# Kernel optimization log

Measured on AMD Instinct MI355X. Metric: run time of the kernel, lower is better.

## Reference

```python
import jax, jax.numpy as jnp
import numpy as np

N_NODES = 100000
N_EDGES = 1600000
D = 128  # h_feats


def setup_inputs() -> dict:
    key = jax.random.key(0)
    k1, k2, k3, k4 = jax.random.split(key, 4)
    x = jax.random.normal(k1, (N_NODES, D), dtype=jnp.float32)
    edge_index = jax.random.randint(k2, (2, N_EDGES), 0, N_NODES, dtype=jnp.int64)
    # Linear(2D -> D), torch layout [out, in]
    W1 = jax.random.normal(k3, (D, 2 * D), dtype=jnp.float32) * (1.0 / np.sqrt(2 * D))
    b1 = jnp.zeros((D,), dtype=jnp.float32)
    # Linear(D -> 1)
    W2 = jax.random.normal(k4, (1, D), dtype=jnp.float32) * (1.0 / np.sqrt(D))
    b2 = jnp.zeros((1,), dtype=jnp.float32)
    return {"x": x, "edge_index": edge_index, "W1": W1, "b1": b1, "W2": W2, "b2": b2}


def reference(x, edge_index, W1, b1, W2, b2):
    # gather both endpoints and concat along features: [E, 2D]
    h = jnp.concatenate([x[edge_index[0]], x[edge_index[1]]], axis=-1)
    h = jax.nn.relu(h @ W1.T + b1)          # [E, D]
    h = h @ W2.T + b2                        # [E, 1]
    return h.squeeze(1)                      # [E]
```

## Files before the change

### kernel.cpp

```cpp
#include <hip/hip_runtime.h>
#include <hip/hip_bf16.h>

#define N_NODES 100000
#define N_EDGES 1600000
#define NT_TILES 1563
#define PRE_BLKX 392

#define BQ_OFF 12800000
#define SA_OFF 25600000
#define SB_OFF 26000000

typedef __attribute__((ext_vector_type(8))) short short8v;
typedef __attribute__((ext_vector_type(4))) float float4v;

__device__ __forceinline__ unsigned short f2bf(float f) {
    unsigned int u = __float_as_uint(f);
    u += 0x7fffu + ((u >> 16) & 1u);
    return (unsigned short)(u >> 16);
}
__device__ __forceinline__ unsigned int pack2bf(float a, float b) {
    return (unsigned int)f2bf(a) | ((unsigned int)f2bf(b) << 16);
}
__device__ __forceinline__ float2 bfpair(unsigned int w) {
    return float2{__uint_as_float(w << 16), __uint_as_float(w & 0xffff0000u)};
}
#define MAGICB 12583040.0f
__device__ __forceinline__ unsigned int qmagic(float f, float inv) {
    return __float_as_uint(fmaf(f, inv, MAGICB));
}

__global__ __launch_bounds__(256) void precompute_kernel(
    const float* __restrict__ x, const float* __restrict__ W1,
    const float* __restrict__ b1, unsigned char* __restrict__ Aq,
    unsigned char* __restrict__ Bq, float* __restrict__ sA,
    float* __restrict__ sB) {
    __shared__ unsigned short wlds[128 * 136];
    __shared__ unsigned short xlds[64 * 136];

    const int tid = threadIdx.x;
    const int by = blockIdx.y;
    unsigned char* __restrict__ Q = by ? Bq : Aq;
    float* __restrict__ S = by ? sB : sA;

    const int wave = tid >> 6;
    const int lane = tid & 63;
    const int quad = lane >> 4;
    const int l15 = lane & 15;

    float4 b1v[2];
#pragma unroll
    for (int j = 0; j < 2; ++j)
        b1v[j] = *reinterpret_cast<const float4*>(b1 + wave * 32 + j * 16 + quad * 4);

#pragma unroll
    for (int i = 0; i < 16; ++i) {
        int fi = tid + i * 256;
        int jl = fi >> 5, c4 = fi & 31;
        float4 w4 = reinterpret_cast<const float4*>(W1)[(size_t)jl * 64 + by * 32 + c4];
        unsigned int* d = reinterpret_cast<unsigned int*>(&wlds[jl * 136 + c4 * 4]);
        d[0] = pack2bf(w4.x, w4.y);
        d[1] = pack2bf(w4.z, w4.w);
    }

    float4 xr[8];
    int t = blockIdx.x;
#pragma unroll
    for (int i = 0; i < 8; ++i) {
        int fi = tid + i * 256;
        int n = fi >> 5, c4 = fi & 31;
        int nn = t * 64 + n; nn = nn < N_NODES ? nn : N_NODES - 1;
        xr[i] = reinterpret_cast<const float4*>(x)[(size_t)nn * 32 + c4];
    }

    for (; t < NT_TILES; t += PRE_BLKX) {
        __syncthreads();
#pragma unroll
        for (int i = 0; i < 8; ++i) {
            int fi = tid + i * 256;
            int n = fi >> 5, c4 = fi & 31;
            unsigned int* d = reinterpret_cast<unsigned int*>(&xlds[n * 136 + c4 * 4]);
            d[0] = pack2bf(xr[i].x, xr[i].y);
            d[1] = pack2bf(xr[i].z, xr[i].w);
        }
        __syncthreads();

        const int tn = t + PRE_BLKX;
        if (tn < NT_TILES) {
#pragma unroll
            for (int i = 0; i < 8; ++i) {
                int fi = tid + i * 256;
                int n = fi >> 5, c4 = fi & 31;
                int nn = tn * 64 + n; nn = nn < N_NODES ? nn : N_NODES - 1;
                xr[i] = reinterpret_cast<const float4*>(x)[(size_t)nn * 32 + c4];
            }
        }

        float4v acc[4][2];
#pragma unroll
        for (int i = 0; i < 4; ++i)
#pragma unroll
            for (int j = 0; j < 2; ++j) acc[i][j] = float4v{0.f, 0.f, 0.f, 0.f};

#pragma unroll
        for (int s = 0; s < 4; ++s) {
            const int k0 = s * 32 + quad * 8;
            short8v wf[2], xf[4];
#pragma unroll
            for (int j = 0; j < 2; ++j)
                wf[j] = *reinterpret_cast<const short8v*>(&wlds[(wave * 32 + j * 16 + l15) * 136 + k0]);
#pragma unroll
            for (int i = 0; i < 4; ++i)
                xf[i] = *reinterpret_cast<const short8v*>(&xlds[(i * 16 + l15) * 136 + k0]);
#pragma unroll
            for (int i = 0; i < 4; ++i)
#pragma unroll
                for (int j = 0; j < 2; ++j)
                    acc[i][j] = __builtin_amdgcn_mfma_f32_16x16x32_bf16(wf[j], xf[i], acc[i][j], 0, 0, 0);
        }
        __syncthreads();

#pragma unroll
        for (int i = 0; i < 4; ++i) {
            const int nl = i * 16 + l15;
#pragma unroll
            for (int j = 0; j < 2; ++j) {
                const int colb = wave * 32 + j * 16 + quad * 4;
                float r0 = acc[i][j][0], r1 = acc[i][j][1];
                float r2 = acc[i][j][2], r3 = acc[i][j][3];
                if (by == 0) {
                    r0 += b1v[j].x; r1 += b1v[j].y;
                    r2 += b1v[j].z; r3 += b1v[j].w;
                }
                uint2 st = {pack2bf(r0, r1), pack2bf(r2, r3)};
                *reinterpret_cast<uint2*>(&xlds[nl * 132 + colb]) = st;
            }
        }
        __syncthreads();

        const int row = tid >> 2, part = tid & 3;
        const int n = t * 64 + row;
        uint4 wv[4];
#pragma unroll
        for (int q = 0; q < 4; ++q)
            wv[q] = *reinterpret_cast<const uint4*>(&xlds[row * 132 + part * 32 + q * 8]);

        float m = 1e-6f;
#pragma unroll
        for (int q = 0; q < 4; ++q) {
            unsigned int ws[4] = {wv[q].x, wv[q].y, wv[q].z, wv[q].w};
#pragma unroll
            for (int w = 0; w < 4; ++w) {
                float2 f = bfpair(ws[w]);
                m = fmaxf(m, fmaxf(fabsf(f.x), fabsf(f.y)));
            }
        }
        m = fmaxf(m, __shfl_xor(m, 1));
        m = fmaxf(m, __shfl_xor(m, 2));
        const float inv = 127.0f / m;

        unsigned int ob[8];
#pragma unroll
        for (int q = 0; q < 4; ++q) {
            unsigned int ws[4] = {wv[q].x, wv[q].y, wv[q].z, wv[q].w};
#pragma unroll
            for (int w = 0; w < 2; ++w) {
                float2 f0 = bfpair(ws[2 * w + 0]);
                float2 f1 = bfpair(ws[2 * w + 1]);
                unsigned int q0 = qmagic(f0.x, inv), q1 = qmagic(f0.y, inv);
                unsigned int q2 = qmagic(f1.x, inv), q3 = qmagic(f1.y, inv);
                ob[q * 2 + w] = (q0 & 0xffu) | ((q1 & 0xffu) << 8) |
                                ((q2 & 0xffu) << 16) | (q3 << 24);
            }
        }
        if (n < N_NODES) {
            uint4 s0 = {ob[0], ob[1], ob[2], ob[3]};
            uint4 s1 = {ob[4], ob[5], ob[6], ob[7]};
            uint4* dst = reinterpret_cast<uint4*>(Q + (size_t)n * 128 + part * 32);
            dst[0] = s0;
            dst[1] = s1;
            if (part == 0) S[n] = m * (1.0f / 127.0f);
        }
    }
}

template <bool IS64>
__device__ __forceinline__ void edge_loop(
    const long long* __restrict__ ei, const unsigned char* __restrict__ Aq,
    const unsigned char* __restrict__ Bq, const float* __restrict__ sA,
    const float* __restrict__ sB, const float* __restrict__ W2, float bias2,
    float* __restrict__ out, int wid, int nwaves, int eg, int sl) {
    const int k0 = sl * 32;
    float w2f[32];
#pragma unroll
    for (int j = 0; j < 8; ++j)
        *reinterpret_cast<float4*>(&w2f[j * 4]) =
            *reinterpret_cast<const float4*>(W2 + k0 + j * 4);
    const int* e32 = reinterpret_cast<const int*>(ei);

    for (int base = wid * 16; base < N_EDGES; base += nwaves * 16) {
        const int e = base + eg;
        int u, v;
        if (IS64) { u = (int)ei[e]; v = (int)ei[N_EDGES + e]; }
        else      { u = e32[e];     v = e32[N_EDGES + e]; }

        const uint4* pa = reinterpret_cast<const uint4*>(Aq + (unsigned)u * 128 + k0);
        const uint4* pb = reinterpret_cast<const uint4*>(Bq + (unsigned)v * 128 + k0);
        uint4 a0 = pa[0], a1 = pa[1];
        uint4 b0 = pb[0], b1w = pb[1];
        const float su = sA[u];
        const float sv = sB[v];
        const float r = sv * __builtin_amdgcn_rcpf(su);
        const float c = fmaf(r, 128.0f, 128.0f);

        unsigned int aw[8] = {a0.x, a0.y, a0.z, a0.w, a1.x, a1.y, a1.z, a1.w};
        unsigned int bw[8] = {b0.x, b0.y, b0.z, b0.w, b1w.x, b1w.y, b1w.z, b1w.w};

        float p = 0.f;
#pragma unroll
        for (int wi = 0; wi < 8; ++wi) {
#pragma unroll
            for (int byt = 0; byt < 4; ++byt) {
                float fa = (float)((aw[wi] >> (8 * byt)) & 0xffu);
                float fb = (float)((bw[wi] >> (8 * byt)) & 0xffu);
                float s = fmaxf(fmaf(fb, r, fa) - c, 0.f);
                p = fmaf(s, w2f[wi * 4 + byt], p);
            }
        }
        p += __shfl_xor(p, 1);
        p += __shfl_xor(p, 2);
        if (sl == 0) out[e] = fmaf(su, p, bias2);
    }
}

__global__ __launch_bounds__(256, 8) void edge_kernel(
    const long long* __restrict__ ei, const unsigned char* __restrict__ Aq,
    const unsigned char* __restrict__ Bq, const float* __restrict__ sA,
    const float* __restrict__ sB, const float* __restrict__ W2,
    const float* __restrict__ b2, float* __restrict__ out) {
    const int lane = threadIdx.x & 63;
    const int eg = lane >> 2;
    const int sl = lane & 3;
    const float bias2 = b2[0];

    const unsigned int hi = reinterpret_cast<const unsigned int*>(ei)[2 * lane + 1];
    const bool is64 = (__ballot(hi != 0) == 0ull);

    const int wid = (int)(((unsigned)(blockIdx.x * blockDim.x + threadIdx.x)) >> 6);
    const int nwaves = (int)(((unsigned)(gridDim.x * blockDim.x)) >> 6);

    if (is64) edge_loop<true>(ei, Aq, Bq, sA, sB, W2, bias2, out, wid, nwaves, eg, sl);
    else      edge_loop<false>(ei, Aq, Bq, sA, sB, W2, bias2, out, wid, nwaves, eg, sl);
}

extern "C" void kernel_launch(void* const* d_in, const int* in_sizes, int n_in,
                              void* d_out, int out_size, void* d_ws, size_t ws_size,
                              hipStream_t stream) {
    const float* x = (const float*)d_in[0];
    const long long* ei = (const long long*)d_in[1];
    const float* W1 = (const float*)d_in[2];
    const float* b1 = (const float*)d_in[3];
    const float* W2 = (const float*)d_in[4];
    const float* b2 = (const float*)d_in[5];
    float* out = (float*)d_out;

    unsigned char* Aq = (unsigned char*)d_ws;
    unsigned char* Bq = (unsigned char*)d_ws + BQ_OFF;
    float* sA = (float*)((char*)d_ws + SA_OFF);
    float* sB = (float*)((char*)d_ws + SB_OFF);

    dim3 g1(PRE_BLKX, 2);
    precompute_kernel<<<g1, 256, 0, stream>>>(x, W1, b1, Aq, Bq, sA, sB);
    edge_kernel<<<2048, 256, 0, stream>>>(ei, Aq, Bq, sA, sB, W2, b2, out);
}
```

Before: 182.3 us.

## Fuse A/B node projections into one block per 32-node tile

The precompute kernel now computes both halves of W1 (the source and destination projections) in one block over 32-node tiles, instead of two grid rows that each reload the same x tile. Each x tile is read from global memory once and feeds 256 output columns, with each wave owning 64 columns. Quantisation is factored into a helper that runs twice per tile, sharing the LDS staging buffer. The cost is a 64KB weight LDS footprint, which limits occupancy, plus extra barriers. The edge kernel's launch-bounds occupancy hint also drops from 8 to 4.

```diff
diff --git a/kernel.cpp b/kernel.cpp
--- a/kernel.cpp
+++ b/kernel.cpp
@@ -3,8 +3,8 @@
 
 #define N_NODES 100000
 #define N_EDGES 1600000
-#define NT_TILES 1563
-#define PRE_BLKX 392
+#define NT32    3125
+#define PRE_BLKS 625
 
 #define BQ_OFF 12800000
 #define SA_OFF 25600000
@@ -27,6 +27,40 @@
 #define MAGICB 12583040.0f
 __device__ __forceinline__ unsigned int qmagic(float f, float inv) {
     return __float_as_uint(fmaf(f, inv, MAGICB));
+}
+
+__device__ __forceinline__ void quant_store(
+    const unsigned short* __restrict__ xlds, unsigned char* __restrict__ Q,
+    float* __restrict__ S, int n0, int tid) {
+    const int row = tid >> 3, part = tid & 7;
+    const unsigned short* src = xlds + row * 132 + part * 16;
+    uint4 w0 = *reinterpret_cast<const uint4*>(src);
+    uint4 w1 = *reinterpret_cast<const uint4*>(src + 8);
+    unsigned int ws[8] = {w0.x, w0.y, w0.z, w0.w, w1.x, w1.y, w1.z, w1.w};
+    float m = 1e-6f;
+#pragma unroll
+    for (int k = 0; k < 8; ++k) {
+        float2 f = bfpair(ws[k]);
+        m = fmaxf(m, fmaxf(fabsf(f.x), fabsf(f.y)));
+    }
+    m = fmaxf(m, __shfl_xor(m, 1));
+    m = fmaxf(m, __shfl_xor(m, 2));
+    m = fmaxf(m, __shfl_xor(m, 4));
+    const float inv = 127.0f / m;
+    unsigned int ob[4];
+#pragma unroll
+    for (int k = 0; k < 4; ++k) {
+        float2 f0 = bfpair(ws[2 * k]);
+        float2 f1 = bfpair(ws[2 * k + 1]);
+        unsigned int q0 = qmagic(f0.x, inv), q1 = qmagic(f0.y, inv);
+        unsigned int q2 = qmagic(f1.x, inv), q3 = qmagic(f1.y, inv);
+        ob[k] = (q0 & 0xffu) | ((q1 & 0xffu) << 8) |
+                ((q2 & 0xffu) << 16) | (q3 << 24);
+    }
+    const int n = n0 + row;
+    *reinterpret_cast<uint4*>(Q + (size_t)n * 128 + part * 16) =
+        uint4{ob[0], ob[1], ob[2], ob[3]};
+    if (part == 0) S[n] = m * (1.0f / 127.0f);
 }
 
 __global__ __launch_bounds__(256) void precompute_kernel(
@@ -34,152 +68,118 @@
     const float* __restrict__ b1, unsigned char* __restrict__ Aq,
     unsigned char* __restrict__ Bq, float* __restrict__ sA,
     float* __restrict__ sB) {
-    __shared__ unsigned short wlds[128 * 136];
-    __shared__ unsigned short xlds[64 * 136];
+    __shared__ unsigned short wlds[256 * 132];
+    __shared__ unsigned short xlds[32 * 132];
 
     const int tid = threadIdx.x;
-    const int by = blockIdx.y;
-    unsigned char* __restrict__ Q = by ? Bq : Aq;
-    float* __restrict__ S = by ? sB : sA;
-
-    const int wave = tid >> 6;
-    const int lane = tid & 63;
-    const int quad = lane >> 4;
-    const int l15 = lane & 15;
-
-    float4 b1v[2];
-#pragma unroll
-    for (int j = 0; j < 2; ++j)
-        b1v[j] = *reinterpret_cast<const float4*>(b1 + wave * 32 + j * 16 + quad * 4);
-
-#pragma unroll
-    for (int i = 0; i < 16; ++i) {
+    const int wave = tid >> 6, lane = tid & 63;
+    const int quad = lane >> 4, l15 = lane & 15;
+
+    float4 b1v[4];
+    if (wave < 2) {
+#pragma unroll
+        for (int j = 0; j < 4; ++j)
+            b1v[j] = *reinterpret_cast<const float4*>(b1 + wave * 64 + j * 16 + quad * 4);
+    }
+
+#pragma unroll
+    for (int i = 0; i < 32; ++i) {
         int fi = tid + i * 256;
-        int jl = fi >> 5, c4 = fi & 31;
-        float4 w4 = reinterpret_cast<const float4*>(W1)[(size_t)jl * 64 + by * 32 + c4];
-        unsigned int* d = reinterpret_cast<unsigned int*>(&wlds[jl * 136 + c4 * 4]);
+        int jc = fi >> 5, c4 = fi & 31;
+        float4 w4 = reinterpret_cast<const float4*>(
+            W1)[(size_t)(jc & 127) * 64 + (jc >> 7) * 32 + c4];
+        unsigned int* d = reinterpret_cast<unsigned int*>(&wlds[jc * 132 + c4 * 4]);
         d[0] = pack2bf(w4.x, w4.y);
         d[1] = pack2bf(w4.z, w4.w);
     }
 
-    float4 xr[8];
+    float4 xr[4];
     int t = blockIdx.x;
 #pragma unroll
-    for (int i = 0; i < 8; ++i) {
+    for (int i = 0; i < 4; ++i) {
         int fi = tid + i * 256;
         int n = fi >> 5, c4 = fi & 31;
-        int nn = t * 64 + n; nn = nn < N_NODES ? nn : N_NODES - 1;
-        xr[i] = reinterpret_cast<const float4*>(x)[(size_t)nn * 32 + c4];
-    }
-
-    for (; t < NT_TILES; t += PRE_BLKX) {
-        __syncthreads();
-#pragma unroll
-        for (int i = 0; i < 8; ++i) {
+        xr[i] = reinterpret_cast<const float4*>(x)[(size_t)(t * 32 + n) * 32 + c4];
+    }
+
+    for (; t < NT32; t += PRE_BLKS) {
+        __syncthreads();
+#pragma unroll
+        for (int i = 0; i < 4; ++i) {
             int fi = tid + i * 256;
             int n = fi >> 5, c4 = fi & 31;
-            unsigned int* d = reinterpret_cast<unsigned int*>(&xlds[n * 136 + c4 * 4]);
+            unsigned int* d = reinterpret_cast<unsigned int*>(&xlds[n * 132 + c4 * 4]);
             d[0] = pack2bf(xr[i].x, xr[i].y);
             d[1] = pack2bf(xr[i].z, xr[i].w);
         }
         __syncthreads();
 
-        const int tn = t + PRE_BLKX;
-        if (tn < NT_TILES) {
-#pragma unroll
-            for (int i = 0; i < 8; ++i) {
+        const int tn = t + PRE_BLKS;
+        if (tn < NT32) {
+#pragma unroll
+            for (int i = 0; i < 4; ++i) {
                 int fi = tid + i * 256;
                 int n = fi >> 5, c4 = fi & 31;
-                int nn = tn * 64 + n; nn = nn < N_NODES ? nn : N_NODES - 1;
-                xr[i] = reinterpret_cast<const float4*>(x)[(size_t)nn * 32 + c4];
+                xr[i] = reinterpret_cast<const float4*>(x)[(size_t)(tn * 32 + n) * 32 + c4];
             }
         }
 
-        float4v acc[4][2];
-#pragma unroll
-        for (int i = 0; i < 4; ++i)
-#pragma unroll
-            for (int j = 0; j < 2; ++j) acc[i][j] = float4v{0.f, 0.f, 0.f, 0.f};
+        float4v acc[2][4];
+#pragma unroll
+        for (int i = 0; i < 2; ++i)
+#pragma unroll
+            for (int j = 0; j < 4; ++j) acc[i][j] = float4v{0.f, 0.f, 0.f, 0.f};
 
 #pragma unroll
         for (int s = 0; s < 4; ++s) {
             const int k0 = s * 32 + quad * 8;
-            short8v wf[2], xf[4];
-#pragma unroll
-            for (int j = 0; j < 2; ++j)
-                wf[j] = *reinterpret_cast<const short8v*>(&wlds[(wave * 32 + j * 16 + l15) * 136 + k0]);
-#pragma unroll
-            for (int i = 0; i < 4; ++i)
-                xf[i] = *reinterpret_cast<const short8v*>(&xlds[(i * 16 + l15) * 136 + k0]);
-#pragma unroll
-            for (int i = 0; i < 4; ++i)
-#pragma unroll
-                for (int j = 0; j < 2; ++j)
+            short8v xf[2], wf[4];
+#pragma unroll
+            for (int i = 0; i < 2; ++i)
+                xf[i] = *reinterpret_cast<const short8v*>(&xlds[(i * 16 + l15) * 132 + k0]);
+#pragma unroll
+            for (int j = 0; j < 4; ++j)
+                wf[j] = *reinterpret_cast<const short8v*>(
+                    &wlds[(wave * 64 + j * 16 + l15) * 132 + k0]);
+#pragma unroll
+            for (int i = 0; i < 2; ++i)
+#pragma unroll
+                for (int j = 0; j < 4; ++j)
                     acc[i][j] = __builtin_amdgcn_mfma_f32_16x16x32_bf16(wf[j], xf[i], acc[i][j], 0, 0, 0);
         }
         __syncthreads();
 
-#pragma unroll
-        for (int i = 0; i < 4; ++i) {
-            const int nl = i * 16 + l15;
-#pragma unroll
-            for (int j = 0; j < 2; ++j) {
-                const int colb = wave * 32 + j * 16 + quad * 4;
-                float r0 = acc[i][j][0], r1 = acc[i][j][1];
-                float r2 = acc[i][j][2], r3 = acc[i][j][3];
-                if (by == 0) {
-                    r0 += b1v[j].x; r1 += b1v[j].y;
-                    r2 += b1v[j].z; r3 += b1v[j].w;
+        if (wave < 2) {
+#pragma unroll
+            for (int i = 0; i < 2; ++i)
+#pragma unroll
+                for (int j = 0; j < 4; ++j) {
+                    const int col = wave * 64 + j * 16 + quad * 4;
+                    float r0 = acc[i][j][0] + b1v[j].x;
+                    float r1 = acc[i][j][1] + b1v[j].y;
+                    float r2 = acc[i][j][2] + b1v[j].z;
+                    float r3 = acc[i][j][3] + b1v[j].w;
+                    uint2 st = {pack2bf(r0, r1), pack2bf(r2, r3)};
+                    *reinterpret_cast<uint2*>(&xlds[(i * 16 + l15) * 132 + col]) = st;
                 }
-                uint2 st = {pack2bf(r0, r1), pack2bf(r2, r3)};
-                *reinterpret_cast<uint2*>(&xlds[nl * 132 + colb]) = st;
-            }
-        }
-        __syncthreads();
-
-        const int row = tid >> 2, part = tid & 3;
-        const int n = t * 64 + row;
-        uint4 wv[4];
-#pragma unroll
-        for (int q = 0; q < 4; ++q)
-            wv[q] = *reinterpret_cast<const uint4*>(&xlds[row * 132 + part * 32 + q * 8]);
-
-        float m = 1e-6f;
-#pragma unroll
-        for (int q = 0; q < 4; ++q) {
-            unsigned int ws[4] = {wv[q].x, wv[q].y, wv[q].z, wv[q].w};
-#pragma unroll
-            for (int w = 0; w < 4; ++w) {
-                float2 f = bfpair(ws[w]);
-                m = fmaxf(m, fmaxf(fabsf(f.x), fabsf(f.y)));
-            }
-        }
-        m = fmaxf(m, __shfl_xor(m, 1));
-        m = fmaxf(m, __shfl_xor(m, 2));
-        const float inv = 127.0f / m;
-
-        unsigned int ob[8];
-#pragma unroll
-        for (int q = 0; q < 4; ++q) {
-            unsigned int ws[4] = {wv[q].x, wv[q].y, wv[q].z, wv[q].w};
-#pragma unroll
-            for (int w = 0; w < 2; ++w) {
-                float2 f0 = bfpair(ws[2 * w + 0]);
-                float2 f1 = bfpair(ws[2 * w + 1]);
-                unsigned int q0 = qmagic(f0.x, inv), q1 = qmagic(f0.y, inv);
-                unsigned int q2 = qmagic(f1.x, inv), q3 = qmagic(f1.y, inv);
-                ob[q * 2 + w] = (q0 & 0xffu) | ((q1 & 0xffu) << 8) |
-                                ((q2 & 0xffu) << 16) | (q3 << 24);
-            }
-        }
-        if (n < N_NODES) {
-            uint4 s0 = {ob[0], ob[1], ob[2], ob[3]};
-            uint4 s1 = {ob[4], ob[5], ob[6], ob[7]};
-            uint4* dst = reinterpret_cast<uint4*>(Q + (size_t)n * 128 + part * 32);
-            dst[0] = s0;
-            dst[1] = s1;
-            if (part == 0) S[n] = m * (1.0f / 127.0f);
-        }
+        }
+        __syncthreads();
+        quant_store(xlds, Aq, sA, t * 32, tid);
+        __syncthreads();
+
+        if (wave >= 2) {
+#pragma unroll
+            for (int i = 0; i < 2; ++i)
+#pragma unroll
+                for (int j = 0; j < 4; ++j) {
+                    const int col = (wave - 2) * 64 + j * 16 + quad * 4;
+                    uint2 st = {pack2bf(acc[i][j][0], acc[i][j][1]),
+                                pack2bf(acc[i][j][2], acc[i][j][3])};
+                    *reinterpret_cast<uint2*>(&xlds[(i * 16 + l15) * 132 + col]) = st;
+                }
+        }
+        __syncthreads();
+        quant_store(xlds, Bq, sB, t * 32, tid);
     }
 }
 
@@ -232,7 +232,7 @@
     }
 }
 
-__global__ __launch_bounds__(256, 8) void edge_kernel(
+__global__ __launch_bounds__(256, 4) void edge_kernel(
     const long long* __restrict__ ei, const unsigned char* __restrict__ Aq,
     const unsigned char* __restrict__ Bq, const float* __restrict__ sA,
     const float* __restrict__ sB, const float* __restrict__ W2,
@@ -268,7 +268,6 @@
     float* sA = (float*)((char*)d_ws + SA_OFF);
     float* sB = (float*)((char*)d_ws + SB_OFF);
 
-    dim3 g1(PRE_BLKX, 2);
-    precompute_kernel<<<g1, 256, 0, stream>>>(x, W1, b1, Aq, Bq, sA, sB);
+    precompute_kernel<<<PRE_BLKS, 256, 0, stream>>>(x, W1, b1, Aq, Bq, sA, sB);
     edge_kernel<<<2048, 256, 0, stream>>>(ei, Aq, Bq, sA, sB, W2, b2, out);
 }
```

After: 183.8 us. Within noise of the previous version (+0.8%).
